# Kernel tuning notes

Hardware: AMD Instinct MI355X
Metric: run time of the kernel (lower is better)

Reference implementation:

```python
import jax, jax.numpy as jnp
import numpy as np

B, N, H, HD = 2, 2048, 16, 64
F = H * HD  # feats = 1024
SQRT_D = float(F) ** 0.5  # module uses sqrt(feats), not sqrt(head_dim)
EPS = 1e-5


def layernorm(x, g, b):
    # LayerNorm over last dim (head_dim), shared gamma/beta across heads
    m = jnp.mean(x, axis=-1, keepdims=True)
    v = jnp.mean(jnp.square(x - m), axis=-1, keepdims=True)
    return (x - m) / jnp.sqrt(v + EPS) * g + b


def setup_inputs() -> dict:
    key = jax.random.key(0)
    ks = jax.random.split(key, 14)
    s = 0.02
    return {
        "x": jax.random.normal(ks[0], (B, N, F), dtype=jnp.float32),
        "ln1_g": jnp.ones((HD,), jnp.float32),
        "ln1_b": jnp.zeros((HD,), jnp.float32),
        "ln2_g": jnp.ones((HD,), jnp.float32),
        "ln2_b": jnp.zeros((HD,), jnp.float32),
        # stacked per-head weights: [H, in, out]
        "wq": jax.random.normal(ks[1], (H, HD, HD), jnp.float32) * s,
        "bq": jnp.zeros((H, HD), jnp.float32),
        "wk": jax.random.normal(ks[2], (H, HD, HD), jnp.float32) * s,
        "bk": jnp.zeros((H, HD), jnp.float32),
        "wv": jax.random.normal(ks[3], (H, HD, HD), jnp.float32) * s,
        "bv": jnp.zeros((H, HD), jnp.float32),
        "wo": jax.random.normal(ks[4], (H, HD, HD), jnp.float32) * s,
        "bo": jnp.zeros((H, HD), jnp.float32),
        "w1": jax.random.normal(ks[5], (H, HD, 4 * HD), jnp.float32) * s,
        "b1": jnp.zeros((H, 4 * HD), jnp.float32),
        "w2": jax.random.normal(ks[6], (H, 4 * HD, HD), jnp.float32) * s,
        "b2": jnp.zeros((H, HD), jnp.float32),
        # Method 0 merge Linear(feats, feats): y = x @ wm + bm
        "wm": jax.random.normal(ks[7], (F, F), jnp.float32) * s,
        "bm": jnp.zeros((F,), jnp.float32),
    }


def reference(x, ln1_g, ln1_b, ln2_g, ln2_b, wq, bq, wk, bk, wv, bv, wo, bo,
              w1, b1, w2, b2, wm, bm):
    b, n, f = x.shape
    x4 = x.reshape(b, n, H, HD)  # [b, n, h, hd]

    # --- Multi-head self attention (per-head linears batched over h) ---
    h1 = layernorm(x4, ln1_g, ln1_b)
    q = jnp.einsum("bnhf,hfg->bnhg", h1, wq) + bq
    k = jnp.einsum("bnhf,hfg->bnhg", h1, wk) + bk
    v = jnp.einsum("bnhf,hfg->bnhg", h1, wv) + bv
    qh = jnp.swapaxes(q, 1, 2)  # [b, h, n, hd]
    kh = jnp.swapaxes(k, 1, 2)
    vh = jnp.swapaxes(v, 1, 2)
    score = jax.nn.softmax(jnp.einsum("bhif,bhjf->bhij", qh, kh) / SQRT_D, axis=-1)
    attn = jnp.einsum("bhij,bhjf->bihf", score, vh)  # [b, n, h, hd]
    attn = jnp.einsum("bnhf,hfg->bnhg", attn, wo) + bo
    out = attn + x4

    # --- Per-head FFN (GELU after BOTH linears, as in source; dropout=0) ---
    h2 = layernorm(out, ln2_g, ln2_b)
    t = jax.nn.gelu(jnp.einsum("bnhf,hfg->bnhg", h2, w1) + b1, approximate=False)
    t = jax.nn.gelu(jnp.einsum("bnhg,hgf->bnhf", t, w2) + b2, approximate=False)
    out = t + out

    # --- Method 0 merge ---
    out = out.reshape(b, n, f)
    out = out @ wm + bm
    return out
```

## Files before the change

kernel.cpp:

```cpp
#include <hip/hip_runtime.h>
#include <hip/hip_bf16.h>
#include <math.h>

#define TOKS 4096
#define NSEQ 2048
#define NH 16
#define DH 64
#define FD 1024

typedef __bf16 bf16_t;
typedef bf16_t bf16x4 __attribute__((ext_vector_type(4)));
typedef bf16_t bf16x8 __attribute__((ext_vector_type(8)));
typedef float f32x4 __attribute__((ext_vector_type(4)));

#define GLL16(gsrc, ldst)                                                        \
    __builtin_amdgcn_global_load_lds(                                            \
        (const __attribute__((address_space(1))) void*)(const void*)(gsrc),      \
        (__attribute__((address_space(3))) void*)(void*)(ldst), 16, 0, 0)

__device__ __forceinline__ float geluf(float x) {
    return 0.5f * x * (1.0f + erff(x * 0.70710678118654752f));
}

__device__ __forceinline__ float fexp2(float x) {
    int i = (int)__builtin_fmaf(x, 8388608.0f, 1065063216.0f);
    return __int_as_float(i);
}

__device__ __forceinline__ float fgelu(float x) {
    float e = fexp2(-2.4554542f * x);
    return x * __builtin_amdgcn_rcpf(1.0f + e);
}

__device__ __forceinline__ int lds_sw(int row, int d) {
    return row * 64 + ((((d >> 3) ^ (row & 7)) & 7) << 3) + (d & 7);
}

__device__ __forceinline__ int vperm(int j) {
    return (j & 32) | ((j & 12) << 1) | ((j & 16) >> 2) | (j & 3);
}

__global__ __launch_bounds__(256) void k_prep(
    const float* __restrict__ wm, const float* __restrict__ w1, const float* __restrict__ w2,
    const float* __restrict__ wq, const float* __restrict__ wk,
    const float* __restrict__ wv, const float* __restrict__ wo,
    bf16_t* __restrict__ wt, bf16_t* __restrict__ w1t, bf16_t* __restrict__ w2t,
    bf16_t* __restrict__ wqt, bf16_t* __restrict__ wkt,
    bf16_t* __restrict__ wvt, bf16_t* __restrict__ wot)
{
    __shared__ bf16_t t[64 * 65];
    const int b = blockIdx.x;
    const int tid = threadIdx.x;
    if (b < 256) {
        const int k0 = (b & 15) * 64, n0 = (b >> 4) * 64;
        #pragma unroll
        for (int it = 0; it < 16; it++) {
            int idx = it * 256 + tid;
            int kk = idx >> 6, nn = idx & 63;
            t[nn * 65 + kk] = (bf16_t)wm[(size_t)(k0 + kk) * FD + n0 + nn];
        }
        __syncthreads();
        #pragma unroll
        for (int it = 0; it < 16; it++) {
            int idx = it * 256 + tid;
            int nn = idx >> 6, kk = idx & 63;
            wt[(size_t)(n0 + nn) * FD + k0 + kk] = t[nn * 65 + kk];
        }
    } else if (b < 320) {
        const int lb = b - 256;
        const int h = lb >> 2, n0 = (lb & 3) * 64;
        const float* src = w1 + (size_t)h * 64 * 256;
        #pragma unroll
        for (int it = 0; it < 16; it++) {
            int idx = it * 256 + tid;
            int kk = idx >> 6, nn = idx & 63;
            t[nn * 65 + kk] = (bf16_t)src[kk * 256 + n0 + nn];
        }
        __syncthreads();
        bf16_t* dst = w1t + (size_t)h * 16384;
        #pragma unroll
        for (int it = 0; it < 16; it++) {
            int idx = it * 256 + tid;
            int nn = idx >> 6, kpos = idx & 63;
            int kb = kpos >> 5, gg = (kpos >> 3) & 3, e = kpos & 7;
            int f = (kb * 2 + (e >> 2)) * 16 + gg * 4 + (e & 3);
            int row = n0 + nn;
            dst[row * 64 + ((((kpos >> 3) ^ (row & 7)) & 7) << 3) + (kpos & 7)] =
                t[nn * 65 + f];
        }
    } else if (b < 384) {
        const int lb = b - 320;
        const int h = lb >> 2, k0 = (lb & 3) * 64;
        const float* src = w2 + (size_t)h * 256 * 64;
        #pragma unroll
        for (int it = 0; it < 16; it++) {
            int idx = it * 256 + tid;
            int kk = idx >> 6, nn = idx & 63;
            t[nn * 65 + kk] = (bf16_t)src[(k0 + kk) * 64 + nn];
        }
        __syncthreads();
        bf16_t* dst = w2t + (size_t)h * 16384;
        #pragma unroll
        for (int it = 0; it < 16; it++) {
            int idx = it * 256 + tid;
            int nn = idx >> 6, kk = idx & 63;
            int c = k0 + vperm(kk);
            int chunk = c >> 3;
            int chunkp = (chunk & 24) | ((chunk ^ nn) & 7);
            dst[nn * 256 + (chunkp << 3) + (c & 7)] = t[nn * 65 + kk];
        }
    } else {
        const int h = b - 384;
        const float* srcs[4] = {wq + h * 4096, wk + h * 4096, wv + h * 4096, wo + h * 4096};
        bf16_t* dsts[4] = {wqt + h * 4096, wkt + h * 4096, wvt + h * 4096, wot + h * 4096};
        #pragma unroll
        for (int m = 0; m < 4; m++) {
            __syncthreads();
            #pragma unroll
            for (int it = 0; it < 16; it++) {
                int idx = it * 256 + tid;
                int ff = idx >> 6, gg = idx & 63;
                t[gg * 65 + ff] = (bf16_t)srcs[m][ff * 64 + gg];
            }
            __syncthreads();
            #pragma unroll
            for (int it = 0; it < 16; it++) {
                int idx = it * 256 + tid;
                int gg = idx >> 6, ff = idx & 63;
                if (m == 3)
                    dsts[m][gg * 64 + ((((ff >> 3) ^ (gg & 7)) & 7) << 3) + (ff & 7)] =
                        t[gg * 65 + ff];
                else
                    dsts[m][gg * 64 + ff] = t[gg * 65 + ff];
            }
        }
    }
}

__global__ __launch_bounds__(256) void k_ln1_qkv(
    const float* __restrict__ x, const float* __restrict__ g1, const float* __restrict__ be1,
    const bf16_t* __restrict__ wqt, const float* __restrict__ bq,
    const bf16_t* __restrict__ wkt, const float* __restrict__ bk,
    const bf16_t* __restrict__ wvt, const float* __restrict__ bv,
    bf16_t* __restrict__ q, bf16_t* __restrict__ k, bf16_t* __restrict__ vt)
{
    __shared__ __align__(16) bf16_t h1s[64 * 64];
    __shared__ __align__(16) bf16_t vts[64 * 72];
    const int h  = blockIdx.y;
    const int t0 = blockIdx.x * 64;
    const int tid = threadIdx.x;

    {
        const int i = tid >> 2, s = tid & 3;
        const float* xr = x + (size_t)(t0 + i) * FD + h * DH + s * 16;
        float vals[16];
        #pragma unroll
        for (int r = 0; r < 4; r++) {
            float4 tmp = *(const float4*)(xr + r * 4);
            vals[r*4+0]=tmp.x; vals[r*4+1]=tmp.y; vals[r*4+2]=tmp.z; vals[r*4+3]=tmp.w;
        }
        float sm = 0.f;
        #pragma unroll
        for (int r = 0; r < 16; r++) sm += vals[r];
        sm += __shfl_xor(sm, 1); sm += __shfl_xor(sm, 2);
        const float mean = sm * (1.0f / 64.0f);
        float vr = 0.f;
        #pragma unroll
        for (int r = 0; r < 16; r++) { float d = vals[r] - mean; vr += d * d; }
        vr += __shfl_xor(vr, 1); vr += __shfl_xor(vr, 2);
        const float rstd = rsqrtf(vr * (1.0f / 64.0f) + 1e-5f);
        bf16x8 o0, o1;
        #pragma unroll
        for (int r = 0; r < 8; r++) {
            int d0 = s * 16 + r, d1 = s * 16 + 8 + r;
            o0[r] = (bf16_t)((vals[r]     - mean) * rstd * g1[d0] + be1[d0]);
            o1[r] = (bf16_t)((vals[8 + r] - mean) * rstd * g1[d1] + be1[d1]);
        }
        *(bf16x8*)&h1s[i * 64 + (((s * 2 + 0) ^ (i & 7)) << 3)] = o0;
        *(bf16x8*)&h1s[i * 64 + (((s * 2 + 1) ^ (i & 7)) << 3)] = o1;
    }
    __syncthreads();

    const int wid = tid >> 6, lane = tid & 63;
    const int g = lane >> 4, c0 = lane & 15;
    const int arow = wid * 16 + c0;

    bf16x8 af0 = *(const bf16x8*)&h1s[arow * 64 + (((g    ) ^ (arow & 7)) << 3)];
    bf16x8 af1 = *(const bf16x8*)&h1s[arow * 64 + (((4 + g) ^ (arow & 7)) << 3)];

    const bf16_t* wqh = wqt + h * 4096;
    const bf16_t* wkh = wkt + h * 4096;
    const bf16_t* wvh = wvt + h * 4096;
    f32x4 aq[4], ak[4], av[4];
    #pragma unroll
    for (int ni = 0; ni < 4; ni++) {
        aq[ni] = (f32x4){0.f, 0.f, 0.f, 0.f};
        ak[ni] = (f32x4){0.f, 0.f, 0.f, 0.f};
        av[ni] = (f32x4){0.f, 0.f, 0.f, 0.f};
    }
    #pragma unroll
    for (int ni = 0; ni < 4; ni++) {
        const int col = ni * 16 + c0;
        bf16x8 b0, b1;
        b0 = *(const bf16x8*)(wqh + col * 64 + g * 8);
        b1 = *(const bf16x8*)(wqh + col * 64 + g * 8 + 32);
        aq[ni] = __builtin_amdgcn_mfma_f32_16x16x32_bf16(af0, b0, aq[ni], 0, 0, 0);
        aq[ni] = __builtin_amdgcn_mfma_f32_16x16x32_bf16(af1, b1, aq[ni], 0, 0, 0);
        b0 = *(const bf16x8*)(wkh + col * 64 + g * 8);
        b1 = *(const bf16x8*)(wkh + col * 64 + g * 8 + 32);
        ak[ni] = __builtin_amdgcn_mfma_f32_16x16x32_bf16(af0, b0, ak[ni], 0, 0, 0);
        ak[ni] = __builtin_amdgcn_mfma_f32_16x16x32_bf16(af1, b1, ak[ni], 0, 0, 0);
        b0 = *(const bf16x8*)(wvh + col * 64 + g * 8);
        b1 = *(const bf16x8*)(wvh + col * 64 + g * 8 + 32);
        av[ni] = __builtin_amdgcn_mfma_f32_16x16x32_bf16(af0, b0, av[ni], 0, 0, 0);
        av[ni] = __builtin_amdgcn_mfma_f32_16x16x32_bf16(af1, b1, av[ni], 0, 0, 0);
    }

    const int rowb = wid * 16 + g * 4;
    const int b = t0 >> 11, n0 = t0 & (NSEQ - 1);
    const size_t qkbase = ((size_t)(b * NH + h) * NSEQ + n0) * DH;

    #pragma unroll
    for (int ni = 0; ni < 4; ni++) {
        const int col = ni * 16 + c0;
        const float bb = bv[h * 64 + col];
        #pragma unroll
        for (int r = 0; r < 4; r++) {
            int i = rowb + r;
            vts[col * 72 + vperm(i)] = (bf16_t)(av[ni][r] + bb);
        }
    }
    __syncthreads();

    #pragma unroll
    for (int ni = 0; ni < 4; ni++) {
        const int col = ni * 16 + c0;
        const float bb = bq[h * 64 + col];
        #pragma unroll
        for (int r = 0; r < 4; r++)
            h1s[lds_sw(rowb + r, col)] = (bf16_t)((aq[ni][r] + bb) * 0.045084220f);
    }
    __syncthreads();
    {
        const int row = tid >> 2, cp = (tid & 3) * 2;
        *(bf16x8*)(q + qkbase + row * DH + cp * 8) =
            *(const bf16x8*)&h1s[row * 64 + ((cp ^ (row & 7)) << 3)];
        *(bf16x8*)(q + qkbase + row * DH + (cp + 1) * 8) =
            *(const bf16x8*)&h1s[row * 64 + (((cp + 1) ^ (row & 7)) << 3)];
        const int d = tid >> 2, c16 = tid & 3;
        size_t vbase = ((size_t)(b * NH + h) * DH + d) * NSEQ + n0 + c16 * 16;
        *(bf16x8*)(vt + vbase)     = *(const bf16x8*)&vts[d * 72 + c16 * 16];
        *(bf16x8*)(vt + vbase + 8) = *(const bf16x8*)&vts[d * 72 + c16 * 16 + 8];
    }
    __syncthreads();

    #pragma unroll
    for (int ni = 0; ni < 4; ni++) {
        const int col = ni * 16 + c0;
        const float bb = bk[h * 64 + col];
        #pragma unroll
        for (int r = 0; r < 4; r++)
            h1s[lds_sw(rowb + r, col)] = (bf16_t)(ak[ni][r] + bb);
    }
    __syncthreads();
    {
        const int row = tid >> 2, cp = (tid & 3) * 2;
        *(bf16x8*)(k + qkbase + row * DH + cp * 8) =
            *(const bf16x8*)&h1s[row * 64 + ((cp ^ (row & 7)) << 3)];
        *(bf16x8*)(k + qkbase + row * DH + (cp + 1) * 8) =
            *(const bf16x8*)&h1s[row * 64 + (((cp + 1) ^ (row & 7)) << 3)];
    }
}

__global__ __launch_bounds__(512, 4) void k_attn(
    const bf16_t* __restrict__ qg, const bf16_t* __restrict__ kg,
    const bf16_t* __restrict__ vt, bf16_t* __restrict__ attnb)
{
    __shared__ __align__(16) bf16_t Ks[2][4096];
    __shared__ __align__(16) bf16_t Vs[2][4096];

    const int bx = blockIdx.x;
    const int bh = ((bx & 7) << 2) | ((bx >> 3) & 3);
    const int qb = blockIdx.y;
    const int tid = threadIdx.x;
    const int wid = tid >> 6, lane = tid & 63;
    const int g = lane >> 4, c0 = lane & 15;
    const int prow = wid * 16 + c0;

    bf16x8 aqf[2];
    {
        const int qrow = qb * 128 + prow;
        const bf16_t* qp = qg + ((size_t)bh * NSEQ + qrow) * DH + g * 8;
        aqf[0] = *(const bf16x8*)qp;
        aqf[1] = *(const bf16x8*)(qp + 32);
    }
    bf16x8 ones;
    #pragma unroll
    for (int e = 0; e < 8; e++) ones[e] = (bf16_t)1.0f;

    int soff[4][2];
    #pragma unroll
    for (int cb = 0; cb < 4; cb++)
        #pragma unroll
        for (int kb = 0; kb < 2; kb++) {
            int row = cb * 16 + c0;
            soff[cb][kb] = row * 64 + (((g + (kb << 2)) ^ (row & 7)) << 3);
        }

    const bf16_t* kbase = kg + (size_t)bh * NSEQ * DH;
    const bf16_t* vbase = vt + (size_t)bh * DH * NSEQ;
    const int lc = wid * 64 + lane;
    const int rowS = lc >> 3, ccS = (lc & 7) ^ (rowS & 7);
    const bf16_t* kp = kbase + rowS * DH + ccS * 8;
    const bf16_t* vp = vbase + (size_t)rowS * NSEQ + ccS * 8;

    GLL16(kp, (char*)&Ks[0][0] + (wid << 10));
    GLL16(vp, (char*)&Vs[0][0] + (wid << 10));
    kp += 64 * DH; vp += 64;

    f32x4 O[4];
    #pragma unroll
    for (int cb = 0; cb < 4; cb++) O[cb] = (f32x4){0.f, 0.f, 0.f, 0.f};
    f32x4 l_acc = (f32x4){0.f, 0.f, 0.f, 0.f};

    auto tile = [&](const bf16_t* Kc, const bf16_t* Vc,
                    bf16_t* Kn, bf16_t* Vn, bool pref) {
        __syncthreads();
        if (pref) {
            GLL16(kp, (char*)Kn + (wid << 10));
            GLL16(vp, (char*)Vn + (wid << 10));
            kp += 64 * DH; vp += 64;
        }

        f32x4 S[4];
        #pragma unroll
        for (int cb = 0; cb < 4; cb++) {
            f32x4 acc = (f32x4){0.f, 0.f, 0.f, 0.f};
            acc = __builtin_amdgcn_mfma_f32_16x16x32_bf16(
                *(const bf16x8*)&Kc[soff[cb][0]], aqf[0], acc, 0, 0, 0);
            acc = __builtin_amdgcn_mfma_f32_16x16x32_bf16(
                *(const bf16x8*)&Kc[soff[cb][1]], aqf[1], acc, 0, 0, 0);
            S[cb] = acc;
        }

        bf16x8 pa0, pa1;
        #pragma unroll
        for (int cb = 0; cb < 2; cb++)
            #pragma unroll
            for (int r = 0; r < 4; r++)
                pa0[cb * 4 + r] = (bf16_t)fexp2(S[cb][r]);
        #pragma unroll
        for (int cb = 0; cb < 2; cb++)
            #pragma unroll
            for (int r = 0; r < 4; r++)
                pa1[cb * 4 + r] = (bf16_t)fexp2(S[2 + cb][r]);

        l_acc = __builtin_amdgcn_mfma_f32_16x16x32_bf16(ones, pa0, l_acc, 0, 0, 0);
        l_acc = __builtin_amdgcn_mfma_f32_16x16x32_bf16(ones, pa1, l_acc, 0, 0, 0);

        #pragma unroll
        for (int cb = 0; cb < 4; cb++) {
            f32x4 acc = O[cb];
            acc = __builtin_amdgcn_mfma_f32_16x16x32_bf16(
                *(const bf16x8*)&Vc[soff[cb][0]], pa0, acc, 0, 0, 0);
            acc = __builtin_amdgcn_mfma_f32_16x16x32_bf16(
                *(const bf16x8*)&Vc[soff[cb][1]], pa1, acc, 0, 0, 0);
            O[cb] = acc;
        }
    };

    #pragma unroll 1
    for (int kt2 = 0; kt2 < 16; kt2++) {
        tile(Ks[0], Vs[0], Ks[1], Vs[1], true);
        tile(Ks[1], Vs[1], Ks[0], Vs[0], kt2 < 15);
    }

    __syncthreads();
    const float inv = 1.0f / l_acc[0];
    bf16_t* Tb = &Ks[0][0];
    #pragma unroll
    for (int cb = 0; cb < 4; cb++)
        #pragma unroll
        for (int r = 0; r < 4; r++) {
            int d = cb * 16 + g * 4 + r;
            Tb[lds_sw(prow, d)] = (bf16_t)(O[cb][r] * inv);
        }
    __syncthreads();
    {
        const int row = tid >> 2, cp = (tid & 3) * 2;
        size_t gbase = ((size_t)bh * NSEQ + qb * 128 + row) * DH;
        *(bf16x8*)(attnb + gbase + cp * 8) =
            *(const bf16x8*)&Tb[row * 64 + ((cp ^ (row & 7)) << 3)];
        *(bf16x8*)(attnb + gbase + (cp + 1) * 8) =
            *(const bf16x8*)&Tb[row * 64 + (((cp + 1) ^ (row & 7)) << 3)];
    }
}

__global__ __launch_bounds__(512, 4) void k_pffn(
    const bf16_t* __restrict__ attnb, const bf16_t* __restrict__ wot,
    const float* __restrict__ bo, const float* __restrict__ x,
    const float* __restrict__ g2, const float* __restrict__ be2,
    const bf16_t* __restrict__ w1t, const float* __restrict__ b1,
    const bf16_t* __restrict__ w2t, const float* __restrict__ b2,
    bf16_t* __restrict__ outp)
{
    __shared__ __align__(16) bf16_t wos[4096];
    __shared__ __align__(16) bf16_t w1s[16384];
    __shared__ __align__(16) bf16_t w2s[16384];
    const int fid = blockIdx.x + 32 * blockIdx.y;
    const int rem = (fid & 7) * 64 + (fid >> 3);
    const int h   = rem >> 5;
    const int t0  = (rem & 31) * 128;
    const int tid = threadIdx.x;
    const int wid = tid >> 6, lane = tid & 63;
    const int g = lane >> 4, c0 = lane & 15;
    const int b = t0 >> 11, n0 = t0 & (NSEQ - 1);
    const int tok = t0 + wid * 16 + c0;

    const bf16_t* ah = attnb + ((size_t)(b * NH + h) * NSEQ + n0) * DH;
    bf16x8 paf0 = *(const bf16x8*)(ah + (wid * 16 + c0) * DH + g * 8);
    bf16x8 paf1 = *(const bf16x8*)(ah + (wid * 16 + c0) * DH + g * 8 + 32);
    float4 xr4[4], bo4[4];
    #pragma unroll
    for (int ni = 0; ni < 4; ni++) {
        xr4[ni] = *(const float4*)(x + (size_t)tok * FD + h * DH + ni * 16 + g * 4);
        bo4[ni] = *(const float4*)(bo + h * DH + ni * 16 + g * 4);
    }

    const bf16_t* s1 = w1t + (size_t)h * 16384;
    const bf16_t* s2 = w2t + (size_t)h * 16384;
    {
        const bf16_t* s0 = wot + h * 4096;
        GLL16(s0 + wid * 512 + lane * 8, (char*)wos + (wid << 10));
        __syncthreads();
    }
    {
        #pragma unroll
        for (int i = 0; i < 4; i++) {
            int grp = wid * 4 + i;
            GLL16(s1 + grp * 512 + lane * 8, (char*)w1s + (grp << 10));
            GLL16(s2 + grp * 512 + lane * 8, (char*)w2s + (grp << 10));
        }
    }

    float o1[4][4];
    #pragma unroll
    for (int ni = 0; ni < 4; ni++) {
        f32x4 acc = (f32x4){0.f, 0.f, 0.f, 0.f};
        const int orow = ni * 16 + c0;
        bf16x8 b0  = *(const bf16x8*)&wos[orow * 64 + (((g    ) ^ (orow & 7)) << 3)];
        bf16x8 b1f = *(const bf16x8*)&wos[orow * 64 + (((4 + g) ^ (orow & 7)) << 3)];
        acc = __builtin_amdgcn_mfma_f32_16x16x32_bf16(b0, paf0, acc, 0, 0, 0);
        acc = __builtin_amdgcn_mfma_f32_16x16x32_bf16(b1f, paf1, acc, 0, 0, 0);
        o1[ni][0] = acc[0] + bo4[ni].x + xr4[ni].x;
        o1[ni][1] = acc[1] + bo4[ni].y + xr4[ni].y;
        o1[ni][2] = acc[2] + bo4[ni].z + xr4[ni].z;
        o1[ni][3] = acc[3] + bo4[ni].w + xr4[ni].w;
    }

    float s = 0.f;
    #pragma unroll
    for (int ni = 0; ni < 4; ni++)
        #pragma unroll
        for (int r = 0; r < 4; r++) s += o1[ni][r];
    s += __shfl_xor(s, 16);
    s += __shfl_xor(s, 32);
    const float mean = s * (1.0f / 64.0f);
    float v = 0.f;
    #pragma unroll
    for (int ni = 0; ni < 4; ni++)
        #pragma unroll
        for (int r = 0; r < 4; r++) { float d = o1[ni][r] - mean; v += d * d; }
    v += __shfl_xor(v, 16);
    v += __shfl_xor(v, 32);
    const float rstd = rsqrtf(v * (1.0f / 64.0f) + 1e-5f);

    bf16x8 hb0, hb1;
    #pragma unroll
    for (int ni = 0; ni < 4; ni++) {
        const float4 g24 = *(const float4*)(g2 + ni * 16 + g * 4);
        const float4 be4 = *(const float4*)(be2 + ni * 16 + g * 4);
        #pragma unroll
        for (int r = 0; r < 4; r++) {
            float hv = (o1[ni][r] - mean) * rstd * ((const float*)&g24)[r]
                       + ((const float*)&be4)[r];
            if (ni < 2) hb0[(ni & 1) * 4 + r] = (bf16_t)hv;
            else        hb1[(ni & 1) * 4 + r] = (bf16_t)hv;
        }
    }
    __syncthreads();

    const float* b1h = b1 + h * 256;
    f32x4 acc2[4];
    #pragma unroll
    for (int nt = 0; nt < 4; nt++) acc2[nt] = (f32x4){0.f, 0.f, 0.f, 0.f};

    #pragma unroll
    for (int ub = 0; ub < 4; ub++) {
        f32x4 a4[4];
        #pragma unroll
        for (int j = 0; j < 4; j++) {
            const int wrow = (ub * 4 + j) * 16 + c0;
            bf16x8 bf0 = *(const bf16x8*)&w1s[wrow * 64 + (((g    ) ^ (wrow & 7)) << 3)];
            bf16x8 bf1 = *(const bf16x8*)&w1s[wrow * 64 + (((4 + g) ^ (wrow & 7)) << 3)];
            f32x4 acc = (f32x4){0.f, 0.f, 0.f, 0.f};
            acc = __builtin_amdgcn_mfma_f32_16x16x32_bf16(bf0, hb0, acc, 0, 0, 0);
            acc = __builtin_amdgcn_mfma_f32_16x16x32_bf16(bf1, hb1, acc, 0, 0, 0);
            a4[j] = acc;
        }
        float4 bb0 = *(const float4*)(b1h + (ub * 4 + 0) * 16 + g * 4);
        float4 bb1 = *(const float4*)(b1h + (ub * 4 + 1) * 16 + g * 4);
        float4 bb2 = *(const float4*)(b1h + (ub * 4 + 2) * 16 + g * 4);
        float4 bb3 = *(const float4*)(b1h + (ub * 4 + 3) * 16 + g * 4);
        bf16x8 p0, p1;
        #pragma unroll
        for (int r = 0; r < 4; r++) {
            p0[r]     = (bf16_t)fgelu(a4[0][r] + ((const float*)&bb0)[r]);
            p0[4 + r] = (bf16_t)fgelu(a4[1][r] + ((const float*)&bb1)[r]);
            p1[r]     = (bf16_t)fgelu(a4[2][r] + ((const float*)&bb2)[r]);
            p1[4 + r] = (bf16_t)fgelu(a4[3][r] + ((const float*)&bb3)[r]);
        }
        #pragma unroll
        for (int nt = 0; nt < 4; nt++) {
            const int vrow = nt * 16 + c0;
            bf16x8 bw0 = *(const bf16x8*)&w2s[vrow * 256 +
                            ((ub * 8 + ((g    ) ^ (vrow & 7))) << 3)];
            bf16x8 bw1 = *(const bf16x8*)&w2s[vrow * 256 +
                            ((ub * 8 + ((g + 4) ^ (vrow & 7))) << 3)];
            acc2[nt] = __builtin_amdgcn_mfma_f32_16x16x32_bf16(bw0, p0, acc2[nt], 0, 0, 0);
            acc2[nt] = __builtin_amdgcn_mfma_f32_16x16x32_bf16(bw1, p1, acc2[nt], 0, 0, 0);
        }
    }

    const float* b2h = b2 + h * 64;
    #pragma unroll
    for (int nt = 0; nt < 4; nt++) {
        const float4 b24 = *(const float4*)(b2h + nt * 16 + g * 4);
        bf16x4 ow;
        ow[0] = (bf16_t)(fgelu(acc2[nt][0] + b24.x) + o1[nt][0]);
        ow[1] = (bf16_t)(fgelu(acc2[nt][1] + b24.y) + o1[nt][1]);
        ow[2] = (bf16_t)(fgelu(acc2[nt][2] + b24.z) + o1[nt][2]);
        ow[3] = (bf16_t)(fgelu(acc2[nt][3] + b24.w) + o1[nt][3]);
        *(bf16x4*)(outp + (size_t)tok * FD + h * DH + nt * 16 + g * 4) = ow;
    }
}

__global__ __launch_bounds__(256) void k_merge(
    const bf16_t* __restrict__ A, const bf16_t* __restrict__ Wt, const float* __restrict__ bias,
    float* __restrict__ C)
{
    __shared__ __align__(16) bf16_t As[128 * 64];
    __shared__ __align__(16) bf16_t Bs[64 * 64];
    const int n0 = blockIdx.x * 64;
    const int m0 = blockIdx.y * 128;
    const int tid = threadIdx.x;
    const int wid = tid >> 6, lane = tid & 63;
    const int c0 = lane & 15, g = lane >> 4;

    const bf16_t* aS[4]; int aO[4];
    #pragma unroll
    for (int i = 0; i < 4; i++) {
        int grp = wid * 4 + i;
        int lc = grp * 64 + lane;
        int row = lc >> 3, cc = (lc & 7) ^ (row & 7);
        aS[i] = A + (size_t)(m0 + row) * FD + cc * 8;
        aO[i] = grp << 10;
    }
    const bf16_t* bS[2]; int bO[2];
    #pragma unroll
    for (int i = 0; i < 2; i++) {
        int grp = wid * 2 + i;
        int lc = grp * 64 + lane;
        int row = lc >> 3, cc = (lc & 7) ^ (row & 7);
        bS[i] = Wt + (size_t)(n0 + row) * FD + cc * 8;
        bO[i] = grp << 10;
    }

    f32x4 acc[2][4];
    #pragma unroll
    for (int mi = 0; mi < 2; mi++)
        #pragma unroll
        for (int ni = 0; ni < 4; ni++)
            acc[mi][ni] = (f32x4){0.f, 0.f, 0.f, 0.f};

    float bv[4];
    #pragma unroll
    for (int ni = 0; ni < 4; ni++) bv[ni] = bias[n0 + ni * 16 + c0];

    for (int k0 = 0; k0 < FD; k0 += 64) {
        __syncthreads();
        #pragma unroll
        for (int i = 0; i < 4; i++) GLL16(aS[i] + k0, (char*)As + aO[i]);
        #pragma unroll
        for (int i = 0; i < 2; i++) GLL16(bS[i] + k0, (char*)Bs + bO[i]);
        __syncthreads();

        bf16x8 af[2][2];
        #pragma unroll
        for (int mi = 0; mi < 2; mi++)
            #pragma unroll
            for (int kk = 0; kk < 2; kk++) {
                int arow = wid * 32 + mi * 16 + c0;
                int ch = kk * 4 + g;
                af[mi][kk] = *(const bf16x8*)&As[arow * 64 + ((ch ^ (arow & 7)) << 3)];
            }
        bf16x8 bfr[4][2];
        #pragma unroll
        for (int ni = 0; ni < 4; ni++)
            #pragma unroll
            for (int kk = 0; kk < 2; kk++) {
                int brow = ni * 16 + c0;
                int ch = kk * 4 + g;
                bfr[ni][kk] = *(const bf16x8*)&Bs[brow * 64 + ((ch ^ (brow & 7)) << 3)];
            }
        #pragma unroll
        for (int mi = 0; mi < 2; mi++)
            #pragma unroll
            for (int ni = 0; ni < 4; ni++)
                #pragma unroll
                for (int kk = 0; kk < 2; kk++)
                    acc[mi][ni] = __builtin_amdgcn_mfma_f32_16x16x32_bf16(
                        af[mi][kk], bfr[ni][kk], acc[mi][ni], 0, 0, 0);
    }

    #pragma unroll
    for (int mi = 0; mi < 2; mi++)
        #pragma unroll
        for (int r = 0; r < 4; r++) {
            int row = m0 + wid * 32 + mi * 16 + g * 4 + r;
            float* cp = C + (size_t)row * FD + n0;
            #pragma unroll
            for (int ni = 0; ni < 4; ni++)
                cp[ni * 16 + c0] = acc[mi][ni][r] + bv[ni];
        }
}

extern "C" void kernel_launch(void* const* d_in, const int* in_sizes, int n_in,
                              void* d_out, int out_size, void* d_ws, size_t ws_size,
                              hipStream_t stream) {
    const float* x   = (const float*)d_in[0];
    const float* g1  = (const float*)d_in[1];
    const float* be1 = (const float*)d_in[2];
    const float* g2  = (const float*)d_in[3];
    const float* be2 = (const float*)d_in[4];
    const float* wq  = (const float*)d_in[5];
    const float* bq  = (const float*)d_in[6];
    const float* wk  = (const float*)d_in[7];
    const float* bk  = (const float*)d_in[8];
    const float* wv  = (const float*)d_in[9];
    const float* bv  = (const float*)d_in[10];
    const float* wo  = (const float*)d_in[11];
    const float* bo  = (const float*)d_in[12];
    const float* w1  = (const float*)d_in[13];
    const float* b1  = (const float*)d_in[14];
    const float* w2  = (const float*)d_in[15];
    const float* b2  = (const float*)d_in[16];
    const float* wm  = (const float*)d_in[17];
    const float* bm  = (const float*)d_in[18];

    char* wsb = (char*)d_ws;
    bf16_t* qb_   = (bf16_t*)(wsb);
    bf16_t* kb_   = (bf16_t*)(wsb + (size_t)8  * 1048576);
    bf16_t* vtb   = (bf16_t*)(wsb + (size_t)16 * 1048576);
    bf16_t* attnb = (bf16_t*)(wsb + (size_t)24 * 1048576);
    bf16_t* out2  = (bf16_t*)(wsb + (size_t)40 * 1048576);
    bf16_t* wtb   = (bf16_t*)(wsb + (size_t)56 * 1048576);
    bf16_t* w1tb  = (bf16_t*)(wsb + (size_t)58 * 1048576);
    bf16_t* w2tb  = (bf16_t*)(wsb + (size_t)58 * 1048576 + 524288);
    bf16_t* wqtb  = (bf16_t*)(wsb + (size_t)59 * 1048576);
    bf16_t* wktb  = (bf16_t*)(wsb + (size_t)59 * 1048576 + 131072);
    bf16_t* wvtb  = (bf16_t*)(wsb + (size_t)59 * 1048576 + 262144);
    bf16_t* wotb  = (bf16_t*)(wsb + (size_t)59 * 1048576 + 393216);

    k_prep<<<dim3(400), 256, 0, stream>>>(wm, w1, w2, wq, wk, wv, wo,
                                          wtb, w1tb, w2tb, wqtb, wktb, wvtb, wotb);
    k_ln1_qkv<<<dim3(TOKS / 64, NH), 256, 0, stream>>>(x, g1, be1, wqtb, bq, wktb, bk, wvtb, bv,
                                                       qb_, kb_, vtb);
    k_attn<<<dim3(32, NSEQ / 128), 512, 0, stream>>>(qb_, kb_, vtb, attnb);
    k_pffn<<<dim3(32, 16), 512, 0, stream>>>(attnb, wotb, bo, x, g2, be2,
                                             w1tb, b1, w2tb, b2, out2);
    k_merge<<<dim3(FD / 64, TOKS / 128), 256, 0, stream>>>(out2, wtb, bm, (float*)d_out);
}
```

Before: 100.7 us.

## Split attention KV range across two blocks and combine partials in FFN kernel

The attention kernel now splits each query tile's key/value sequence into two halves handled by separate blocks. This doubles the grid from 512 to 1024 blocks to fill more of the per-CU block slots that the launch bounds allow. Each block writes an unnormalized bf16 output partial and its row-sum. The following FFN kernel adds the two partials and divides by the combined sum before its first matmul. In exchange it adds extra global traffic for the doubled partial buffer and the row sums, and an extra bf16 rounding of unnormalized partials.

```diff
diff --git a/kernel.cpp b/kernel.cpp
--- a/kernel.cpp
+++ b/kernel.cpp
@@ -274,14 +274,15 @@
 
 __global__ __launch_bounds__(512, 4) void k_attn(
     const bf16_t* __restrict__ qg, const bf16_t* __restrict__ kg,
-    const bf16_t* __restrict__ vt, bf16_t* __restrict__ attnb)
+    const bf16_t* __restrict__ vt, bf16_t* __restrict__ opart, float* __restrict__ lp)
 {
     __shared__ __align__(16) bf16_t Ks[2][4096];
     __shared__ __align__(16) bf16_t Vs[2][4096];
 
     const int bx = blockIdx.x;
     const int bh = ((bx & 7) << 2) | ((bx >> 3) & 3);
-    const int qb = blockIdx.y;
+    const int qb = blockIdx.y & 15;
+    const int jh = blockIdx.y >> 4;
     const int tid = threadIdx.x;
     const int wid = tid >> 6, lane = tid & 63;
     const int g = lane >> 4, c0 = lane & 15;
@@ -307,8 +308,8 @@
             soff[cb][kb] = row * 64 + (((g + (kb << 2)) ^ (row & 7)) << 3);
         }
 
-    const bf16_t* kbase = kg + (size_t)bh * NSEQ * DH;
-    const bf16_t* vbase = vt + (size_t)bh * DH * NSEQ;
+    const bf16_t* kbase = kg + (size_t)bh * NSEQ * DH + (size_t)jh * 1024 * DH;
+    const bf16_t* vbase = vt + (size_t)bh * DH * NSEQ + jh * 1024;
     const int lc = wid * 64 + lane;
     const int rowS = lc >> 3, ccS = (lc & 7) ^ (rowS & 7);
     const bf16_t* kp = kbase + rowS * DH + ccS * 8;
@@ -370,34 +371,37 @@
     };
 
     #pragma unroll 1
-    for (int kt2 = 0; kt2 < 16; kt2++) {
+    for (int kt2 = 0; kt2 < 8; kt2++) {
         tile(Ks[0], Vs[0], Ks[1], Vs[1], true);
-        tile(Ks[1], Vs[1], Ks[0], Vs[0], kt2 < 15);
+        tile(Ks[1], Vs[1], Ks[0], Vs[0], kt2 < 7);
     }
 
     __syncthreads();
-    const float inv = 1.0f / l_acc[0];
     bf16_t* Tb = &Ks[0][0];
     #pragma unroll
     for (int cb = 0; cb < 4; cb++)
         #pragma unroll
         for (int r = 0; r < 4; r++) {
             int d = cb * 16 + g * 4 + r;
-            Tb[lds_sw(prow, d)] = (bf16_t)(O[cb][r] * inv);
-        }
+            Tb[lds_sw(prow, d)] = (bf16_t)(O[cb][r]);
+        }
+    if (g == 0)
+        lp[((size_t)jh * 32 + bh) * NSEQ + qb * 128 + prow] = l_acc[0];
     __syncthreads();
     {
         const int row = tid >> 2, cp = (tid & 3) * 2;
-        size_t gbase = ((size_t)bh * NSEQ + qb * 128 + row) * DH;
-        *(bf16x8*)(attnb + gbase + cp * 8) =
+        size_t gbase = (size_t)jh * (32ull * NSEQ * DH)
+                     + ((size_t)bh * NSEQ + qb * 128 + row) * DH;
+        *(bf16x8*)(opart + gbase + cp * 8) =
             *(const bf16x8*)&Tb[row * 64 + ((cp ^ (row & 7)) << 3)];
-        *(bf16x8*)(attnb + gbase + (cp + 1) * 8) =
+        *(bf16x8*)(opart + gbase + (cp + 1) * 8) =
             *(const bf16x8*)&Tb[row * 64 + (((cp + 1) ^ (row & 7)) << 3)];
     }
 }
 
 __global__ __launch_bounds__(512, 4) void k_pffn(
-    const bf16_t* __restrict__ attnb, const bf16_t* __restrict__ wot,
+    const bf16_t* __restrict__ opart, const float* __restrict__ lp,
+    const bf16_t* __restrict__ wot,
     const float* __restrict__ bo, const float* __restrict__ x,
     const float* __restrict__ g2, const float* __restrict__ be2,
     const bf16_t* __restrict__ w1t, const float* __restrict__ b1,
@@ -417,14 +421,27 @@
     const int b = t0 >> 11, n0 = t0 & (NSEQ - 1);
     const int tok = t0 + wid * 16 + c0;
 
-    const bf16_t* ah = attnb + ((size_t)(b * NH + h) * NSEQ + n0) * DH;
-    bf16x8 paf0 = *(const bf16x8*)(ah + (wid * 16 + c0) * DH + g * 8);
-    bf16x8 paf1 = *(const bf16x8*)(ah + (wid * 16 + c0) * DH + g * 8 + 32);
+    const int rowin = n0 + wid * 16 + c0;
+    const size_t bhN = (size_t)(b * NH + h) * NSEQ;
+    const bf16_t* o0p = opart + (bhN + rowin) * DH;
+    const bf16_t* o1p = o0p + 32ull * NSEQ * DH;
+    bf16x8 q00 = *(const bf16x8*)(o0p + g * 8);
+    bf16x8 q01 = *(const bf16x8*)(o0p + g * 8 + 32);
+    bf16x8 q10 = *(const bf16x8*)(o1p + g * 8);
+    bf16x8 q11 = *(const bf16x8*)(o1p + g * 8 + 32);
+    const float lsum = lp[bhN + rowin] + lp[32ull * NSEQ + bhN + rowin];
     float4 xr4[4], bo4[4];
     #pragma unroll
     for (int ni = 0; ni < 4; ni++) {
         xr4[ni] = *(const float4*)(x + (size_t)tok * FD + h * DH + ni * 16 + g * 4);
         bo4[ni] = *(const float4*)(bo + h * DH + ni * 16 + g * 4);
+    }
+    const float inv = 1.0f / lsum;
+    bf16x8 paf0, paf1;
+    #pragma unroll
+    for (int e = 0; e < 8; e++) {
+        paf0[e] = (bf16_t)(((float)q00[e] + (float)q10[e]) * inv);
+        paf1[e] = (bf16_t)(((float)q01[e] + (float)q11[e]) * inv);
     }
 
     const bf16_t* s1 = w1t + (size_t)h * 16384;
@@ -662,8 +679,9 @@
     bf16_t* qb_   = (bf16_t*)(wsb);
     bf16_t* kb_   = (bf16_t*)(wsb + (size_t)8  * 1048576);
     bf16_t* vtb   = (bf16_t*)(wsb + (size_t)16 * 1048576);
-    bf16_t* attnb = (bf16_t*)(wsb + (size_t)24 * 1048576);
+    bf16_t* opart = (bf16_t*)(wsb + (size_t)24 * 1048576);
     bf16_t* out2  = (bf16_t*)(wsb + (size_t)40 * 1048576);
+    float*  lpart = (float*)(wsb + (size_t)48 * 1048576);
     bf16_t* wtb   = (bf16_t*)(wsb + (size_t)56 * 1048576);
     bf16_t* w1tb  = (bf16_t*)(wsb + (size_t)58 * 1048576);
     bf16_t* w2tb  = (bf16_t*)(wsb + (size_t)58 * 1048576 + 524288);
@@ -676,8 +694,8 @@
                                           wtb, w1tb, w2tb, wqtb, wktb, wvtb, wotb);
     k_ln1_qkv<<<dim3(TOKS / 64, NH), 256, 0, stream>>>(x, g1, be1, wqtb, bq, wktb, bk, wvtb, bv,
                                                        qb_, kb_, vtb);
-    k_attn<<<dim3(32, NSEQ / 128), 512, 0, stream>>>(qb_, kb_, vtb, attnb);
-    k_pffn<<<dim3(32, 16), 512, 0, stream>>>(attnb, wotb, bo, x, g2, be2,
+    k_attn<<<dim3(32, 32), 512, 0, stream>>>(qb_, kb_, vtb, opart, lpart);
+    k_pffn<<<dim3(32, 16), 512, 0, stream>>>(opart, lpart, wotb, bo, x, g2, be2,
                                              w1tb, b1, w2tb, b2, out2);
     k_merge<<<dim3(FD / 64, TOKS / 128), 256, 0, stream>>>(out2, wtb, bm, (float*)d_out);
 }
```

After: 103.6 us. +2.8%, slower.
